# Kernel tuning notes

Measured on AMD Instinct MI355X. Metric: run time of the kernel, lower is better.

The kernel has to match this reference:

```python
import jax, jax.numpy as jnp
from jax import lax
import numpy as np

B, C, T = 8, 512, 8192
RATIO = 2
K = 12  # filter taps for both up and down FIR


def kaiser_sinc_filter1d(cutoff, half_width, kernel_size):
    # Faithful port of BigVGAN's kaiser_sinc_filter1d (even kernel_size path)
    half_size = kernel_size // 2
    delta_f = 4.0 * half_width
    A = 2.285 * (half_size - 1) * np.pi * delta_f + 7.95
    if A > 50.0:
        beta = 0.1102 * (A - 8.7)
    elif A >= 21.0:
        beta = 0.5842 * (A - 21.0) ** 0.4 + 0.07886 * (A - 21.0)
    else:
        beta = 0.0
    window = np.kaiser(kernel_size, beta)
    time = np.arange(-half_size, half_size) + 0.5  # even kernel
    filt = 2.0 * cutoff * window * np.sinc(2.0 * cutoff * time)
    filt = filt / filt.sum()
    return jnp.asarray(filt, dtype=jnp.float32)


def setup_inputs() -> dict:
    key = jax.random.key(0)
    k1, k2 = jax.random.split(key)
    x = jax.random.normal(k1, (B, C, T), dtype=jnp.float32)
    # Snake per-channel alpha parameter in LOG scale (alpha_logscale=True)
    alpha = 0.1 * jax.random.normal(k2, (C,), dtype=jnp.float32)
    # Fixed anti-aliasing low-pass filters (buffers)
    up_filter = kaiser_sinc_filter1d(cutoff=0.5 / RATIO, half_width=0.6 / RATIO, kernel_size=K)
    down_filter = kaiser_sinc_filter1d(cutoff=0.5 / RATIO, half_width=0.6 / RATIO, kernel_size=K)
    return {"x": x, "alpha": alpha, "up_filter": up_filter, "down_filter": down_filter}


def _forward(x, alpha, up_filter, down_filter):
    Bc, Cc, Tc = x.shape
    dn = ("NCH", "OIH", "NCH")
    # ---- UpSample1d: replicate-pad, grouped conv_transpose (stride=RATIO), crop ----
    pad = K // RATIO - 1                                  # 5
    pad_left = pad * RATIO + (K - RATIO) // 2             # 15
    pad_right = pad * RATIO + (K - RATIO + 1) // 2        # 15
    xp = jnp.pad(x, ((0, 0), (0, 0), (pad, pad)), mode="edge")
    w_up = jnp.broadcast_to(up_filter[None, None, :], (Cc, 1, K))
    # conv_transpose1d(stride=s) == input-dilated conv with flipped kernel, full padding
    y = RATIO * lax.conv_general_dilated(
        xp, jnp.flip(w_up, axis=-1),
        window_strides=(1,), padding=[(K - 1, K - 1)],
        lhs_dilation=(RATIO,), dimension_numbers=dn,
        feature_group_count=Cc)
    y = y[..., pad_left:-pad_right]                       # [B, C, RATIO*T]
    # ---- Snake activation (logscale alpha) ----
    a = jnp.exp(alpha)[None, :, None]
    y = y + (1.0 / (a + 1e-9)) * jnp.square(jnp.sin(a * y))
    # ---- DownSample1d: replicate-pad, grouped strided FIR conv ----
    dpl = K // 2 - 1                                       # 5 (even kernel)
    dpr = K // 2                                           # 6
    yp = jnp.pad(y, ((0, 0), (0, 0), (dpl, dpr)), mode="edge")
    w_dn = jnp.broadcast_to(down_filter[None, None, :], (Cc, 1, K))
    out = lax.conv_general_dilated(
        yp, w_dn,
        window_strides=(RATIO,), padding=[(0, 0)],
        dimension_numbers=dn, feature_group_count=Cc)
    return out                                             # [B, C, T]


def reference(x, alpha, up_filter, down_filter):
    return _forward(x, alpha, up_filter, down_filter)
```

## Files before the change

kernel.cpp:

```cpp
#include <hip/hip_runtime.h>

#define T_LEN 8192
#define C_N   512
#define BLOCK 256
#define OPT   8
#define TCHUNK (BLOCK * OPT)
#define NCHUNK 4
#define INV_2PI 0.15915494309189535f

typedef float f32x2 __attribute__((ext_vector_type(2)));


__global__ __launch_bounds__(BLOCK, 8) void act1d_fused(
    const float* __restrict__ x,
    const float* __restrict__ alpha,
    const float* __restrict__ wup_g,
    const float* __restrict__ wdn_g,
    float* __restrict__ out)
{
    const int bx    = blockIdx.x;
    const int chunk = bx & (NCHUNK - 1);
    const int bc    = bx >> 2;
    const int c     = bc & (C_N - 1);
    const int tid   = threadIdx.x;
    const int lane  = tid & 63;
    const int N     = chunk * TCHUNK + OPT * tid;
    const int N63   = N + OPT * (63 - lane);

    const float* __restrict__ xrow = x   + (size_t)bc * T_LEN;
    float*       __restrict__ orow = out + (size_t)bc * T_LEN;

    float xr[16];
    if (N >= 8) {
#pragma unroll
        for (int w = 0; w < 4; ++w) {
            const float4 t4 = *reinterpret_cast<const float4*>(xrow + N - 8 + 4 * w);
            xr[4 * w + 0] = t4.x;
            xr[4 * w + 1] = t4.y;
            xr[4 * w + 2] = t4.z;
            xr[4 * w + 3] = t4.w;
        }
    } else {
#pragma unroll
        for (int u = 0; u < 16; ++u)
            xr[u] = xrow[max(N - 8 + u, 0)];
    }

    const int s_  = lane >> 1;
    const int par = lane & 1;
    const int hb  = N63 + 2 + s_ + par;
    float xt[6];
    if (N63 + 12 < T_LEN) {
#pragma unroll
        for (int j = 0; j < 6; ++j)
            xt[j] = xrow[hb + j];
    } else {
#pragma unroll
        for (int j = 0; j < 6; ++j)
            xt[j] = xrow[min(hb + j, T_LEN - 1)];
    }

    f32x2 cpair[6], dpair[6];
#pragma unroll
    for (int t = 0; t < 6; ++t) {
        cpair[t] = (f32x2){ wup_g[2 * t + 1] + wup_g[2 * t + 1],
                            wup_g[2 * t]     + wup_g[2 * t] };
        dpair[t] = (f32x2){ wdn_g[2 * t + 1], wdn_g[2 * t] };
    }
    const float a     = __expf(alpha[c]);
    const float inv_a = 1.0f / (a + 1e-9f);
    const float ka    = a * INV_2PI;
    const f32x2 ka2   = (f32x2){ ka, ka };
    const f32x2 inva2 = (f32x2){ inv_a, inv_a };

    f32x2 A[14];
#pragma unroll
    for (int p = 1; p <= 8; ++p)
        A[p] = (f32x2){ 0.0f, 0.0f };
#pragma unroll
    for (int u = 3; u <= 15; ++u) {
        const f32x2 su = (f32x2){ xr[u], xr[u] };
#pragma unroll
        for (int t = 0; t < 6; ++t) {
            const int p = u - 7 + t;
            if (p >= 1 && p <= 8)
                A[p] = __builtin_elementwise_fma(cpair[t], su, A[p]);
        }
    }

    float yh = 0.0f;
#pragma unroll
    for (int j = 0; j < 6; ++j) {
        const float cj = par ? cpair[5 - j].y : cpair[5 - j].x;
        yh = fmaf(cj, xt[j], yh);
    }
    {
        const float s = __builtin_amdgcn_sinf(ka * yh);
        yh = fmaf(s * s, inv_a, yh);
    }

#pragma unroll
    for (int p = 1; p <= 8; ++p) {
        const f32x2 arg = A[p] * ka2;
        const f32x2 s   = (f32x2){ __builtin_amdgcn_sinf(arg.x),
                                   __builtin_amdgcn_sinf(arg.y) };
        A[p] = __builtin_elementwise_fma(s * s, inva2, A[p]);
    }

    if (N == 0) {
        const float v = A[3].x;
        A[1] = (f32x2){ v, v };
        A[2] = (f32x2){ v, v };
        A[3].y = v;
    }

    const bool is63 = (lane == 63);
#pragma unroll
    for (int p = 1; p <= 5; ++p) {
        const float dx = __shfl_down(A[p].x, 1, 64);
        const float dy = __shfl_down(A[p].y, 1, 64);
        const float gx = __int_as_float(
            __builtin_amdgcn_readlane(__float_as_int(yh), 2 * p));
        const float gy = __int_as_float(
            __builtin_amdgcn_readlane(__float_as_int(yh), 2 * p - 1));
        A[8 + p] = (f32x2){ is63 ? gx : dx, is63 ? gy : dy };
    }

    if (N == T_LEN - OPT) {
        const float h5 = A[11].y;
        A[11] = (f32x2){ h5, h5 };
        A[12] = (f32x2){ h5, h5 };
        A[13] = (f32x2){ h5, h5 };
    }

    float o[OPT];
#pragma unroll
    for (int r = 0; r < OPT; ++r) {
        f32x2 P = dpair[0] * A[r + 1];
#pragma unroll
        for (int j = 1; j < 6; ++j)
            P = __builtin_elementwise_fma(dpair[j], A[r + j + 1], P);
        o[r] = P.x + P.y;
    }

    *reinterpret_cast<float4*>(orow + N)     = make_float4(o[0], o[1], o[2], o[3]);
    *reinterpret_cast<float4*>(orow + N + 4) = make_float4(o[4], o[5], o[6], o[7]);
}

extern "C" void kernel_launch(void* const* d_in, const int* in_sizes, int n_in,
                              void* d_out, int out_size, void* d_ws, size_t ws_size,
                              hipStream_t stream)
{
    const float* x     = (const float*)d_in[0];
    const float* alpha = (const float*)d_in[1];
    const float* wup   = (const float*)d_in[2];
    const float* wdn   = (const float*)d_in[3];
    float*       out   = (float*)d_out;

    const int B_N  = out_size / (C_N * T_LEN);
    const int grid = B_N * C_N * NCHUNK;

    act1d_fused<<<grid, BLOCK, 0, stream>>>(x, alpha, wup, wdn, out);
}
```

Before: 48.96 us.

## Process all time chunks per block with register-prefetched next chunk input

Each block now handles a whole (batch, channel) row, looping over the four time chunks instead of launching one block per chunk. The next chunk's input window is loaded into registers before the current chunk's compute, so the load latency can overlap with arithmetic. Per-row setup (filters, alpha, exp) is also amortized across chunks. This cuts the grid to a quarter of the blocks and lowers the occupancy hint from 8 to 5 to leave room for the extra registers, which may reduce latency hiding and parallelism.

```diff
diff --git a/kernel.cpp b/kernel.cpp
--- a/kernel.cpp
+++ b/kernel.cpp
@@ -11,53 +11,38 @@
 typedef float f32x2 __attribute__((ext_vector_type(2)));
 
 
-__global__ __launch_bounds__(BLOCK, 8) void act1d_fused(
+__global__ __launch_bounds__(BLOCK, 5) void act1d_fused(
     const float* __restrict__ x,
     const float* __restrict__ alpha,
     const float* __restrict__ wup_g,
     const float* __restrict__ wdn_g,
     float* __restrict__ out)
 {
-    const int bx    = blockIdx.x;
-    const int chunk = bx & (NCHUNK - 1);
-    const int bc    = bx >> 2;
-    const int c     = bc & (C_N - 1);
-    const int tid   = threadIdx.x;
-    const int lane  = tid & 63;
-    const int N     = chunk * TCHUNK + OPT * tid;
-    const int N63   = N + OPT * (63 - lane);
+    const int bc   = blockIdx.x;
+    const int c    = bc & (C_N - 1);
+    const int tid  = threadIdx.x;
+    const int lane = tid & 63;
 
     const float* __restrict__ xrow = x   + (size_t)bc * T_LEN;
     float*       __restrict__ orow = out + (size_t)bc * T_LEN;
 
     float xr[16];
-    if (N >= 8) {
+    {
+        const int N = OPT * tid;
+        if (N >= 8) {
 #pragma unroll
-        for (int w = 0; w < 4; ++w) {
-            const float4 t4 = *reinterpret_cast<const float4*>(xrow + N - 8 + 4 * w);
-            xr[4 * w + 0] = t4.x;
-            xr[4 * w + 1] = t4.y;
-            xr[4 * w + 2] = t4.z;
-            xr[4 * w + 3] = t4.w;
+            for (int w = 0; w < 4; ++w) {
+                const float4 t4 = *reinterpret_cast<const float4*>(xrow + N - 8 + 4 * w);
+                xr[4 * w + 0] = t4.x;
+                xr[4 * w + 1] = t4.y;
+                xr[4 * w + 2] = t4.z;
+                xr[4 * w + 3] = t4.w;
+            }
+        } else {
+#pragma unroll
+            for (int u = 0; u < 16; ++u)
+                xr[u] = xrow[max(N - 8 + u, 0)];
         }
-    } else {
-#pragma unroll
-        for (int u = 0; u < 16; ++u)
-            xr[u] = xrow[max(N - 8 + u, 0)];
-    }
-
-    const int s_  = lane >> 1;
-    const int par = lane & 1;
-    const int hb  = N63 + 2 + s_ + par;
-    float xt[6];
-    if (N63 + 12 < T_LEN) {
-#pragma unroll
-        for (int j = 0; j < 6; ++j)
-            xt[j] = xrow[hb + j];
-    } else {
-#pragma unroll
-        for (int j = 0; j < 6; ++j)
-            xt[j] = xrow[min(hb + j, T_LEN - 1)];
     }
 
     f32x2 cpair[6], dpair[6];
@@ -73,78 +58,118 @@
     const f32x2 ka2   = (f32x2){ ka, ka };
     const f32x2 inva2 = (f32x2){ inv_a, inv_a };
 
-    f32x2 A[14];
+    const int s_  = lane >> 1;
+    const int par = lane & 1;
+
 #pragma unroll
-    for (int p = 1; p <= 8; ++p)
-        A[p] = (f32x2){ 0.0f, 0.0f };
+    for (int chunk = 0; chunk < NCHUNK; ++chunk) {
+        const int N   = chunk * TCHUNK + OPT * tid;
+        const int N63 = chunk * TCHUNK + OPT * (tid - lane + 63);
+
+        const int hb = N63 + 2 + s_ + par;
+        float xt[6];
+        if (N63 + 12 < T_LEN) {
 #pragma unroll
-    for (int u = 3; u <= 15; ++u) {
-        const f32x2 su = (f32x2){ xr[u], xr[u] };
+            for (int j = 0; j < 6; ++j)
+                xt[j] = xrow[hb + j];
+        } else {
 #pragma unroll
-        for (int t = 0; t < 6; ++t) {
-            const int p = u - 7 + t;
-            if (p >= 1 && p <= 8)
-                A[p] = __builtin_elementwise_fma(cpair[t], su, A[p]);
+            for (int j = 0; j < 6; ++j)
+                xt[j] = xrow[min(hb + j, T_LEN - 1)];
+        }
+
+        float xrN[16];
+        if (chunk < NCHUNK - 1) {
+            const float* pn = xrow + (chunk + 1) * TCHUNK + OPT * tid - 8;
+#pragma unroll
+            for (int w = 0; w < 4; ++w) {
+                const float4 t4 = *reinterpret_cast<const float4*>(pn + 4 * w);
+                xrN[4 * w + 0] = t4.x;
+                xrN[4 * w + 1] = t4.y;
+                xrN[4 * w + 2] = t4.z;
+                xrN[4 * w + 3] = t4.w;
+            }
+        }
+
+        f32x2 A[14];
+#pragma unroll
+        for (int p = 1; p <= 8; ++p)
+            A[p] = (f32x2){ 0.0f, 0.0f };
+#pragma unroll
+        for (int u = 3; u <= 15; ++u) {
+            const f32x2 su = (f32x2){ xr[u], xr[u] };
+#pragma unroll
+            for (int t = 0; t < 6; ++t) {
+                const int p = u - 7 + t;
+                if (p >= 1 && p <= 8)
+                    A[p] = __builtin_elementwise_fma(cpair[t], su, A[p]);
+            }
+        }
+
+        float yh = 0.0f;
+#pragma unroll
+        for (int j = 0; j < 6; ++j) {
+            const float cj = par ? cpair[5 - j].y : cpair[5 - j].x;
+            yh = fmaf(cj, xt[j], yh);
+        }
+        {
+            const float s = __builtin_amdgcn_sinf(ka * yh);
+            yh = fmaf(s * s, inv_a, yh);
+        }
+
+#pragma unroll
+        for (int p = 1; p <= 8; ++p) {
+            const f32x2 arg = A[p] * ka2;
+            const f32x2 s   = (f32x2){ __builtin_amdgcn_sinf(arg.x),
+                                       __builtin_amdgcn_sinf(arg.y) };
+            A[p] = __builtin_elementwise_fma(s * s, inva2, A[p]);
+        }
+
+        if (N == 0) {
+            const float v = A[3].x;
+            A[1] = (f32x2){ v, v };
+            A[2] = (f32x2){ v, v };
+            A[3].y = v;
+        }
+
+        const bool is63 = (lane == 63);
+#pragma unroll
+        for (int p = 1; p <= 5; ++p) {
+            const float dx = __shfl_down(A[p].x, 1, 64);
+            const float dy = __shfl_down(A[p].y, 1, 64);
+            const float gx = __int_as_float(
+                __builtin_amdgcn_readlane(__float_as_int(yh), 2 * p));
+            const float gy = __int_as_float(
+                __builtin_amdgcn_readlane(__float_as_int(yh), 2 * p - 1));
+            A[8 + p] = (f32x2){ is63 ? gx : dx, is63 ? gy : dy };
+        }
+
+        if (N == T_LEN - OPT) {
+            const float h5 = A[11].y;
+            A[11] = (f32x2){ h5, h5 };
+            A[12] = (f32x2){ h5, h5 };
+            A[13] = (f32x2){ h5, h5 };
+        }
+
+        float o[OPT];
+#pragma unroll
+        for (int r = 0; r < OPT; ++r) {
+            f32x2 P = dpair[0] * A[r + 1];
+#pragma unroll
+            for (int j = 1; j < 6; ++j)
+                P = __builtin_elementwise_fma(dpair[j], A[r + j + 1], P);
+            o[r] = P.x + P.y;
+        }
+
+        *reinterpret_cast<float4*>(orow + N)     = make_float4(o[0], o[1], o[2], o[3]);
+        *reinterpret_cast<float4*>(orow + N + 4) = make_float4(o[4], o[5], o[6], o[7]);
+
+        if (chunk < NCHUNK - 1) {
+#pragma unroll
+            for (int u = 0; u < 16; ++u)
+                xr[u] = xrN[u];
         }
     }
-
-    float yh = 0.0f;
-#pragma unroll
-    for (int j = 0; j < 6; ++j) {
-        const float cj = par ? cpair[5 - j].y : cpair[5 - j].x;
-        yh = fmaf(cj, xt[j], yh);
-    }
-    {
-        const float s = __builtin_amdgcn_sinf(ka * yh);
-        yh = fmaf(s * s, inv_a, yh);
-    }
-
-#pragma unroll
-    for (int p = 1; p <= 8; ++p) {
-        const f32x2 arg = A[p] * ka2;
-        const f32x2 s   = (f32x2){ __builtin_amdgcn_sinf(arg.x),
-                                   __builtin_amdgcn_sinf(arg.y) };
-        A[p] = __builtin_elementwise_fma(s * s, inva2, A[p]);
-    }
-
-    if (N == 0) {
-        const float v = A[3].x;
-        A[1] = (f32x2){ v, v };
-        A[2] = (f32x2){ v, v };
-        A[3].y = v;
-    }
-
-    const bool is63 = (lane == 63);
-#pragma unroll
-    for (int p = 1; p <= 5; ++p) {
-        const float dx = __shfl_down(A[p].x, 1, 64);
-        const float dy = __shfl_down(A[p].y, 1, 64);
-        const float gx = __int_as_float(
-            __builtin_amdgcn_readlane(__float_as_int(yh), 2 * p));
-        const float gy = __int_as_float(
-            __builtin_amdgcn_readlane(__float_as_int(yh), 2 * p - 1));
-        A[8 + p] = (f32x2){ is63 ? gx : dx, is63 ? gy : dy };
-    }
-
-    if (N == T_LEN - OPT) {
-        const float h5 = A[11].y;
-        A[11] = (f32x2){ h5, h5 };
-        A[12] = (f32x2){ h5, h5 };
-        A[13] = (f32x2){ h5, h5 };
-    }
-
-    float o[OPT];
-#pragma unroll
-    for (int r = 0; r < OPT; ++r) {
-        f32x2 P = dpair[0] * A[r + 1];
-#pragma unroll
-        for (int j = 1; j < 6; ++j)
-            P = __builtin_elementwise_fma(dpair[j], A[r + j + 1], P);
-        o[r] = P.x + P.y;
-    }
-
-    *reinterpret_cast<float4*>(orow + N)     = make_float4(o[0], o[1], o[2], o[3]);
-    *reinterpret_cast<float4*>(orow + N + 4) = make_float4(o[4], o[5], o[6], o[7]);
 }
 
 extern "C" void kernel_launch(void* const* d_in, const int* in_sizes, int n_in,
@@ -158,7 +183,7 @@
     float*       out   = (float*)d_out;
 
     const int B_N  = out_size / (C_N * T_LEN);
-    const int grid = B_N * C_N * NCHUNK;
+    const int grid = B_N * C_N;
 
     act1d_fused<<<grid, BLOCK, 0, stream>>>(x, alpha, wup, wdn, out);
 }
```

After: 48.61 us. No clear change (-0.7%).
